# Performance work log

Hardware: AMD Instinct MI355X
Metric: run time of the kernel (lower is better)

The kernel has to match this reference:

```python
import jax, jax.numpy as jnp
import numpy as np

B, IN, OUT, TDIM, YDIM = 4096, 48, 64, 128, 64
HID = OUT * OUT  # 4096, Y_layer hidden/output width


def setup_inputs() -> dict:
    key = jax.random.key(0)
    ks = jax.random.split(key, 9)
    x = jax.random.normal(ks[0], (B, IN, IN), dtype=jnp.float32)
    # symmetrize so input is SPD-like (module assumes SPD inputs)
    x = 0.5 * (x + jnp.swapaxes(x, 1, 2))
    t = jax.random.normal(ks[1], (B, TDIM), dtype=jnp.float32)
    Y = jax.random.normal(ks[2], (B, YDIM), dtype=jnp.float32)
    # Stiefel (orthogonal) weight [input_size(=OUT after increase), output_size]
    W, _ = jnp.linalg.qr(jax.random.normal(ks[3], (OUT, OUT), dtype=jnp.float32))
    # Y_layer MLP params: Linear(YDIM,HID) -> SiLU -> Linear(HID,HID)
    Y_W1 = jax.random.normal(ks[4], (YDIM, HID), dtype=jnp.float32) / np.sqrt(YDIM)
    Y_b1 = jnp.zeros((HID,), dtype=jnp.float32)
    Y_W2 = jax.random.normal(ks[5], (HID, HID), dtype=jnp.float32) / np.sqrt(HID)
    Y_b2 = jnp.zeros((HID,), dtype=jnp.float32)
    return {"input": x, "t": t, "Y": Y, "W": W,
            "Y_W1": Y_W1, "Y_b1": Y_b1, "Y_W2": Y_W2, "Y_b2": Y_b2}


def reference(input, t, Y, W, Y_W1, Y_b1, Y_W2, Y_b2):
    # Y_layer MLP -> per-sample transform emb_Y [B, OUT, OUT]
    h = jax.nn.silu(Y @ Y_W1 + Y_b1)
    emb_Y = (h @ Y_W2 + Y_b2).reshape(B, OUT, OUT)
    # SPDIncreaseDim: embed input in top-left of OUTxOUT, ones on padded diagonal
    pad = OUT - IN
    xp = jnp.pad(input, ((0, 0), (0, pad), (0, pad)))
    add_diag = jnp.concatenate([jnp.zeros(IN, input.dtype), jnp.ones(pad, input.dtype)])
    xp = xp + jnp.diag(add_diag)[None]
    # congruence with Stiefel weight: W^T X W
    out = jnp.einsum('ji,bjk,kl->bil', W, xp, W)
    # congruence with MLP-generated weight: emb_Y X emb_Y^T
    out = jnp.einsum('bij,bjk,blk->bil', emb_Y, out, emb_Y)
    return out
```

## Files before the change

### kernel.cpp

```cpp
#include <hip/hip_runtime.h>
#include <hip/hip_bf16.h>

typedef __bf16 bf16;
typedef __bf16 bf16x8 __attribute__((ext_vector_type(8)));
typedef float floatx4 __attribute__((ext_vector_type(4)));

#define MFMA16(a, b, c) __builtin_amdgcn_mfma_f32_16x16x32_bf16((a), (b), (c), 0, 0, 0)

__device__ inline void gload_lds16(const void* g, void* l) {
    __builtin_amdgcn_global_load_lds((__attribute__((address_space(1))) void*)g,
                                     (__attribute__((address_space(3))) void*)l, 16, 0, 0);
}

__global__ __launch_bounds__(256) void prep_fused(
    const float* __restrict__ W2,
    const float* __restrict__ W,
    const float* __restrict__ b2,
    const float* __restrict__ Y,
    const float* __restrict__ W1,
    const float* __restrict__ b1,
    bf16* __restrict__ W2fT,
    float* __restrict__ b2f,
    bf16* __restrict__ h)
{
    __shared__ __align__(16) char smem[45056];
    int t = threadIdx.x, bid = blockIdx.x;
    int w = t >> 6, l = t & 63;
    int lm = l & 15, q2 = l >> 4, q8 = q2 * 8;

    if (bid < 2048) {
        int pt = bid & 31, i = bid >> 5;
        bf16* sW = (bf16*)smem;
        bf16* sA = sW + 64 * 72;
        bf16* sT = sA + 128 * 72;
        int p0 = pt * 128;

#pragma unroll
        for (int kk = 0; kk < 16; kk++) {
            int idx = t + 256 * kk;
            sW[(idx >> 6) * 72 + (idx & 63)] = (bf16)W[idx];
        }
        {
            const float* src = W2 + (size_t)p0 * 4096 + i * 64;
#pragma unroll
            for (int kk = 0; kk < 8; kk++) {
                int c = t + 256 * kk;
                int row = c >> 4, j4 = (c & 15) * 4;
                float4 v = *(const float4*)(src + (size_t)row * 4096 + j4);
                bf16 tmp[4] = {(bf16)v.x, (bf16)v.y, (bf16)v.z, (bf16)v.w};
                *(uint2*)(sA + row * 72 + j4) = *(const uint2*)tmp;
            }
        }
        __syncthreads();

        floatx4 acc[2][4] = {};
#pragma unroll
        for (int kc = 0; kc < 2; kc++) {
            bf16x8 a0 = *(const bf16x8*)(sA + (w * 32 + lm) * 72 + kc * 32 + q8);
            bf16x8 a1 = *(const bf16x8*)(sA + (w * 32 + 16 + lm) * 72 + kc * 32 + q8);
#pragma unroll
            for (int jn = 0; jn < 4; jn++) {
                bf16x8 bf_ = *(const bf16x8*)(sW + (jn * 16 + lm) * 72 + kc * 32 + q8);
                acc[0][jn] = MFMA16(a0, bf_, acc[0][jn]);
                acc[1][jn] = MFMA16(a1, bf_, acc[1][jn]);
            }
        }
#pragma unroll
        for (int im = 0; im < 2; im++)
#pragma unroll
            for (int jn = 0; jn < 4; jn++) {
                int pr = w * 32 + im * 16 + q2 * 4;
                int lc = jn * 16 + lm;
                union { bf16 h4[4]; uint2 u; } pk;
#pragma unroll
                for (int r = 0; r < 4; r++) pk.h4[r] = (bf16)acc[im][jn][r];
                *(uint2*)(sT + lc * 136 + pr) = pk.u;
            }
        __syncthreads();
#pragma unroll
        for (int kk = 0; kk < 4; kk++) {
            int c = t + 256 * kk;
            int row = c >> 4, off = (c & 15) * 8;
            uint4 v = *(const uint4*)(sT + row * 136 + off);
            *(uint4*)(W2fT + (size_t)(i * 64 + row) * 4096 + p0 + off) = v;
        }
        return;
    }

    if (bid < 2112) {
        int i = bid - 2048;
        if (t < 64) {
            float acc = 0.f;
            const float* b2r = b2 + i * 64;
            const float* wr_ = W + t * 64;
#pragma unroll
            for (int j = 0; j < 64; j++) acc = fmaf(b2r[j], wr_[j], acc);
            b2f[i * 64 + t] = acc;
        }
        return;
    }

    {
        int q = bid - 2112;
        int m0 = (q >> 5) * 128, n0 = (q & 31) * 128;
        bf16* sY = (bf16*)smem;
        bf16* sWT = sY + 128 * 72;

#pragma unroll
        for (int kk = 0; kk < 8; kk++) {
            int c = t + 256 * kk;
            int row = c >> 4, c4 = (c & 15) * 4;
            float4 v = *(const float4*)(Y + (size_t)(m0 + row) * 64 + c4);
            bf16 tmp[4] = {(bf16)v.x, (bf16)v.y, (bf16)v.z, (bf16)v.w};
            *(uint2*)(sY + row * 72 + c4) = *(const uint2*)tmp;
        }
#pragma unroll
        for (int kk = 0; kk < 8; kk++) {
            int c = t + 256 * kk;
            int k = c >> 5, j4 = (c & 31) * 4;
            float4 v = *(const float4*)(W1 + (size_t)k * 4096 + n0 + j4);
            sWT[(j4 + 0) * 72 + k] = (bf16)v.x;
            sWT[(j4 + 1) * 72 + k] = (bf16)v.y;
            sWT[(j4 + 2) * 72 + k] = (bf16)v.z;
            sWT[(j4 + 3) * 72 + k] = (bf16)v.w;
        }
        __syncthreads();

        int wn = (w & 1) * 64, wm = (w >> 1) * 64;
        floatx4 acc[4][4] = {};
#pragma unroll
        for (int kc = 0; kc < 2; kc++) {
            bf16x8 af[4], bfr[4];
#pragma unroll
            for (int i = 0; i < 4; i++)
                af[i] = *(const bf16x8*)(sWT + (wn + i * 16 + lm) * 72 + kc * 32 + q8);
#pragma unroll
            for (int j = 0; j < 4; j++)
                bfr[j] = *(const bf16x8*)(sY + (wm + j * 16 + lm) * 72 + kc * 32 + q8);
#pragma unroll
            for (int i = 0; i < 4; i++)
#pragma unroll
                for (int j = 0; j < 4; j++)
                    acc[i][j] = MFMA16(af[i], bfr[j], acc[i][j]);
        }
#pragma unroll
        for (int i = 0; i < 4; i++) {
            int nb = n0 + wn + i * 16 + q2 * 4;
            float4 bv = *(const float4*)(b1 + nb);
            float bb[4] = {bv.x, bv.y, bv.z, bv.w};
#pragma unroll
            for (int j = 0; j < 4; j++) {
                int m = m0 + wm + j * 16 + lm;
                union { bf16 h4[4]; uint2 u; } pk;
#pragma unroll
                for (int r = 0; r < 4; r++) {
                    float v = acc[i][j][r] + bb[r];
                    v = v / (1.f + __expf(-v));
                    pk.h4[r] = (bf16)v;
                }
                *(uint2*)(h + (size_t)m * 4096 + nb) = pk.u;
            }
        }
    }
}

#define GT 128
#define GK 32
__global__ __launch_bounds__(256, 4) void gemm_bt_bias(
    const bf16* __restrict__ A, const bf16* __restrict__ BT,
    const float* __restrict__ bias, bf16* __restrict__ C,
    int M, int N, int K)
{
    __shared__ bf16 sA[2][GT * GK];
    __shared__ bf16 sB[2][GT * GK];
    int t = threadIdx.x, w = t >> 6, l = t & 63;

    int bid = blockIdx.x;
    int xcd = bid & 7, local = bid >> 3;
    int mt = xcd * 4 + (local & 3);
    int nt = local >> 2;
    int m0 = mt * GT, n0 = nt * GT;

    int lm = l & 15;
    int q2 = l >> 4;
    int soff = ((q2 - (l & 3)) & 3) * 8;
    int wr = (w >> 1) * 64, wc = (w & 1) * 64;

    int rowA = (w * 64 + l) >> 2;
    int ko = (((l & 3) + rowA) & 3) * 8;
    const bf16* pa = A + (size_t)(m0 + rowA) * K + ko;
    const bf16* pb = BT + (size_t)(n0 + rowA) * K + ko;
    const int base0 = (w * 64) * 8, base1 = (w * 64 + 256) * 8;

    floatx4 acc[4][4] = {};

    auto issue = [&](int buf, const bf16* a, const bf16* b) {
        gload_lds16(a, &sA[buf][base0]);
        gload_lds16(a + (size_t)64 * K, &sA[buf][base1]);
        gload_lds16(b, &sB[buf][base0]);
        gload_lds16(b + (size_t)64 * K, &sB[buf][base1]);
    };

    const int KT = K / GK;
    issue(0, pa, pb);
    pa += GK; pb += GK;
    __syncthreads();

    for (int kt = 0; kt < KT; ++kt) {
        int cur = kt & 1;
        if (kt + 1 < KT) {
            issue(cur ^ 1, pa, pb);
            pa += GK; pb += GK;
        }
        const bf16* LA = sA[cur];
        const bf16* LB = sB[cur];
        bf16x8 af[4], bfr[4];
#pragma unroll
        for (int i = 0; i < 4; i++)
            af[i] = *(const bf16x8*)(LA + (wr + i * 16 + lm) * GK + soff);
#pragma unroll
        for (int j = 0; j < 4; j++)
            bfr[j] = *(const bf16x8*)(LB + (wc + j * 16 + lm) * GK + soff);
#pragma unroll
        for (int i = 0; i < 4; i++)
#pragma unroll
            for (int j = 0; j < 4; j++)
                acc[i][j] = MFMA16(af[i], bfr[j], acc[i][j]);
        __syncthreads();
    }

#pragma unroll
    for (int i = 0; i < 4; i++) {
        int r0 = m0 + wr + i * 16 + (l >> 4) * 4;
#pragma unroll
        for (int j = 0; j < 4; j++) {
            int cc = n0 + wc + j * 16 + lm;
            float bb = bias[cc];
#pragma unroll
            for (int r = 0; r < 4; r++)
                C[(size_t)(r0 + r) * N + cc] = (bf16)(acc[i][j][r] + bb);
        }
    }
}

#define ST 72
__global__ __launch_bounds__(256) void batched_congruence(
    const float* __restrict__ x,
    const bf16* __restrict__ F,
    float* __restrict__ out)
{
    __shared__ bf16 sX[64 * ST], sF[64 * ST], sT[64 * ST];
    int t = threadIdx.x, w = t >> 6, l = t & 63;
    int b = blockIdx.x;
    int lm = l & 15, q2 = l >> 4, q8 = q2 * 8;
    int r0 = (w >> 1) * 32, c0 = (w & 1) * 32;

    const float4* xb = (const float4*)(x + (size_t)b * 2304);
    float4 v0 = xb[t];
    float4 v1 = xb[t + 256];
    float4 v2 = (t < 64) ? xb[t + 512] : make_float4(0.f, 0.f, 0.f, 0.f);

    {
        const uint4* gf = (const uint4*)(F + (size_t)b * 4096);
#pragma unroll
        for (int kk = 0; kk < 2; kk++) {
            int c = t + 256 * kk;
            *(uint4*)(sF + (c >> 3) * ST + (c & 7) * 8) = gf[c];
        }
    }
    {
        unsigned* sx32 = (unsigned*)sX;
#pragma unroll
        for (int kk = 0; kk < 4; kk++) {
            int idx = t + 256 * kk;
            if (idx < 384) {
                int r = idx >> 3, d = 24 + (idx & 7);
                sx32[r * 36 + d] = 0u;
            } else if (idx < 896) {
                int k2 = idx - 384;
                int r = 48 + (k2 >> 5), d = k2 & 31;
                unsigned val = 0u;
                if (d == (r >> 1)) val = (r & 1) ? 0x3F800000u : 0x00003F80u;
                sx32[r * 36 + d] = val;
            }
        }
    }
    {
        int c = t;
        bf16 p4[4];
        p4[0] = (bf16)v0.x; p4[1] = (bf16)v0.y; p4[2] = (bf16)v0.z; p4[3] = (bf16)v0.w;
        *(uint2*)(sX + (c / 12) * ST + (c % 12) * 4) = *(const uint2*)p4;
        c = t + 256;
        p4[0] = (bf16)v1.x; p4[1] = (bf16)v1.y; p4[2] = (bf16)v1.z; p4[3] = (bf16)v1.w;
        *(uint2*)(sX + (c / 12) * ST + (c % 12) * 4) = *(const uint2*)p4;
        if (t < 64) {
            c = t + 512;
            p4[0] = (bf16)v2.x; p4[1] = (bf16)v2.y; p4[2] = (bf16)v2.z; p4[3] = (bf16)v2.w;
            *(uint2*)(sX + (c / 12) * ST + (c % 12) * 4) = *(const uint2*)p4;
        }
    }
    __syncthreads();

    auto mm = [&](const bf16* PA, const bf16* PB, floatx4 acc[2][2]) {
#pragma unroll
        for (int kc = 0; kc < 2; kc++) {
            bf16x8 a0 = *(const bf16x8*)(PA + (r0 + lm) * ST + kc * 32 + q8);
            bf16x8 a1 = *(const bf16x8*)(PA + (r0 + 16 + lm) * ST + kc * 32 + q8);
            bf16x8 b0 = *(const bf16x8*)(PB + (c0 + lm) * ST + kc * 32 + q8);
            bf16x8 b1 = *(const bf16x8*)(PB + (c0 + 16 + lm) * ST + kc * 32 + q8);
            acc[0][0] = MFMA16(a0, b0, acc[0][0]);
            acc[0][1] = MFMA16(a0, b1, acc[0][1]);
            acc[1][0] = MFMA16(a1, b0, acc[1][0]);
            acc[1][1] = MFMA16(a1, b1, acc[1][1]);
        }
    };

    floatx4 z = {0.f, 0.f, 0.f, 0.f};
    {
        floatx4 acc[2][2] = {{z, z}, {z, z}};
        mm(sX, sF, acc);
#pragma unroll
        for (int i = 0; i < 2; i++)
#pragma unroll
            for (int j = 0; j < 2; j++) {
                int R = r0 + i * 16 + q2 * 4;
                int Cc = c0 + j * 16 + lm;
                union { bf16 h4[4]; uint2 u; } pk;
#pragma unroll
                for (int r = 0; r < 4; r++) pk.h4[r] = (bf16)acc[i][j][r];
                *(uint2*)(sT + Cc * ST + R) = pk.u;
            }
    }
    __syncthreads();
    {
        floatx4 acc[2][2] = {{z, z}, {z, z}};
        mm(sT, sF, acc);
        float* ob = out + (size_t)b * 4096;
#pragma unroll
        for (int i = 0; i < 2; i++)
#pragma unroll
            for (int j = 0; j < 2; j++) {
                int R = r0 + i * 16 + q2 * 4;
                int Cc = c0 + j * 16 + lm;
#pragma unroll
                for (int r = 0; r < 4; r++)
                    out[(size_t)b * 4096 + (size_t)(R + r) * 64 + Cc] = acc[i][j][r];
            }
        (void)ob;
    }
}

extern "C" void kernel_launch(void* const* d_in, const int* in_sizes, int n_in,
                              void* d_out, int out_size, void* d_ws, size_t ws_size,
                              hipStream_t stream) {
    const float* x  = (const float*)d_in[0];
    const float* Y  = (const float*)d_in[2];
    const float* W  = (const float*)d_in[3];
    const float* W1 = (const float*)d_in[4];
    const float* b1 = (const float*)d_in[5];
    const float* W2 = (const float*)d_in[6];
    const float* b2 = (const float*)d_in[7];
    float* out = (float*)d_out;

    const size_t NN = (size_t)4096 * 4096;
    bf16* h    = (bf16*)d_ws;
    bf16* W2fT = h + NN;
    bf16* emb  = W2fT + NN;
    float* b2f = (float*)d_out;

    prep_fused<<<3136, 256, 0, stream>>>(W2, W, b2, Y, W1, b1, W2fT, b2f, h);
    gemm_bt_bias<<<1024, 256, 0, stream>>>(h, W2fT, b2f, emb, 4096, 4096, 4096);
    batched_congruence<<<4096, 256, 0, stream>>>(x, emb, out);
}
```

Baseline: 332.2 us.

## Fuse bias GEMM and batched congruence into one cooperative kernel with grid sync

Merges the large bf16 GEMM that produces the per-sample transforms and the per-sample congruence into one cooperative kernel, separated by a grid-wide sync. After the sync each block handles four samples and prefetches the next sample's input and transform while computing the current one. This removes a kernel launch and lets the congruence phase start right after the GEMM. The final output store becomes a vectorized transposed float4 write, which relies on the result being symmetric. It depends on all 1024 blocks being co-resident, and falls back to the two separate kernels if the cooperative launch fails.

```diff
diff --git a/kernel.cpp b/kernel.cpp
--- a/kernel.cpp
+++ b/kernel.cpp
@@ -1,5 +1,6 @@
 #include <hip/hip_runtime.h>
 #include <hip/hip_bf16.h>
+#include <hip/hip_cooperative_groups.h>
 
 typedef __bf16 bf16;
 typedef __bf16 bf16x8 __attribute__((ext_vector_type(8)));
@@ -12,16 +13,13 @@
                                      (__attribute__((address_space(3))) void*)l, 16, 0, 0);
 }
 
+#define ST 72
+
 __global__ __launch_bounds__(256) void prep_fused(
-    const float* __restrict__ W2,
-    const float* __restrict__ W,
-    const float* __restrict__ b2,
-    const float* __restrict__ Y,
-    const float* __restrict__ W1,
-    const float* __restrict__ b1,
-    bf16* __restrict__ W2fT,
-    float* __restrict__ b2f,
-    bf16* __restrict__ h)
+    const float* __restrict__ W2, const float* __restrict__ W,
+    const float* __restrict__ b2, const float* __restrict__ Y,
+    const float* __restrict__ W1, const float* __restrict__ b1,
+    bf16* __restrict__ W2fT, float* __restrict__ b2f, bf16* __restrict__ h)
 {
     __shared__ __align__(16) char smem[45056];
     int t = threadIdx.x, bid = blockIdx.x;
@@ -164,63 +162,239 @@
     }
 }
 
-#define GT 128
-#define GK 32
+__global__ __launch_bounds__(256, 4) void gemm_cong(
+    const bf16* __restrict__ A, const bf16* __restrict__ BT,
+    const float* __restrict__ bias, bf16* __restrict__ C,
+    const float* __restrict__ x, float* __restrict__ out)
+{
+    __shared__ __align__(16) char smem[32768];
+    int t = threadIdx.x, w = t >> 6, l = t & 63;
+    int bid = blockIdx.x;
+    int lm = l & 15, q2 = l >> 4, q8 = q2 * 8;
+
+    int s0 = bid * 4;
+    const float4* xb0 = (const float4*)(x + (size_t)s0 * 2304);
+    float4 v0 = xb0[t];
+    float4 v1 = xb0[t + 256];
+    float4 v2 = (t < 64) ? xb0[t + 512] : make_float4(0.f, 0.f, 0.f, 0.f);
+
+    {
+        bf16* sA = (bf16*)smem;
+        bf16* sB = (bf16*)(smem + 16384);
+        int xcd = bid & 7, local = bid >> 3;
+        int mt = xcd * 4 + (local & 3), nt = local >> 2;
+        int m0 = mt * 128, n0 = nt * 128;
+        int soff = ((q2 - (l & 3)) & 3) * 8;
+        int wr = (w >> 1) * 64, wc = (w & 1) * 64;
+        int rowA = (w * 64 + l) >> 2;
+        int ko = (((l & 3) + rowA) & 3) * 8;
+        const bf16* pa = A + (size_t)(m0 + rowA) * 4096 + ko;
+        const bf16* pb = BT + (size_t)(n0 + rowA) * 4096 + ko;
+        const int base0 = (w * 64) * 8, base1 = (w * 64 + 256) * 8;
+
+        floatx4 acc[4][4] = {};
+
+        auto issue = [&](int buf, const bf16* a, const bf16* b) {
+            gload_lds16(a, sA + buf * 4096 + base0);
+            gload_lds16(a + (size_t)64 * 4096, sA + buf * 4096 + base1);
+            gload_lds16(b, sB + buf * 4096 + base0);
+            gload_lds16(b + (size_t)64 * 4096, sB + buf * 4096 + base1);
+        };
+
+        issue(0, pa, pb);
+        pa += 32; pb += 32;
+        __syncthreads();
+
+        for (int kt = 0; kt < 128; ++kt) {
+            int cur = kt & 1;
+            if (kt + 1 < 128) {
+                issue(cur ^ 1, pa, pb);
+                pa += 32; pb += 32;
+            }
+            const bf16* LA = sA + cur * 4096;
+            const bf16* LB = sB + cur * 4096;
+            bf16x8 af[4], bfr[4];
+#pragma unroll
+            for (int i = 0; i < 4; i++)
+                af[i] = *(const bf16x8*)(LA + (wr + i * 16 + lm) * 32 + soff);
+#pragma unroll
+            for (int j = 0; j < 4; j++)
+                bfr[j] = *(const bf16x8*)(LB + (wc + j * 16 + lm) * 32 + soff);
+#pragma unroll
+            for (int i = 0; i < 4; i++)
+#pragma unroll
+                for (int j = 0; j < 4; j++)
+                    acc[i][j] = MFMA16(af[i], bfr[j], acc[i][j]);
+            __syncthreads();
+        }
+
+#pragma unroll
+        for (int i = 0; i < 4; i++) {
+            int r0g = m0 + wr + i * 16 + q2 * 4;
+#pragma unroll
+            for (int j = 0; j < 4; j++) {
+                int cc = n0 + wc + j * 16 + lm;
+                float bb = bias[cc];
+#pragma unroll
+                for (int r = 0; r < 4; r++)
+                    C[(size_t)(r0g + r) * 4096 + cc] = (bf16)(acc[i][j][r] + bb);
+            }
+        }
+    }
+
+    __threadfence();
+    cooperative_groups::this_grid().sync();
+
+    {
+        bf16* sX = (bf16*)smem;
+        bf16* sF = (bf16*)(smem + 9216);
+        bf16* sT = (bf16*)(smem + 18432);
+        int r0 = (w >> 1) * 32, c0 = (w & 1) * 32;
+
+        const uint4* gf0 = (const uint4*)(C + (size_t)s0 * 4096);
+        uint4 f0 = gf0[t], f1 = gf0[t + 256];
+
+        auto mm = [&](const bf16* PA, const bf16* PB, floatx4 acc2[2][2]) {
+#pragma unroll
+            for (int kc = 0; kc < 2; kc++) {
+                bf16x8 a0 = *(const bf16x8*)(PA + (r0 + lm) * ST + kc * 32 + q8);
+                bf16x8 a1 = *(const bf16x8*)(PA + (r0 + 16 + lm) * ST + kc * 32 + q8);
+                bf16x8 b0 = *(const bf16x8*)(PB + (c0 + lm) * ST + kc * 32 + q8);
+                bf16x8 b1 = *(const bf16x8*)(PB + (c0 + 16 + lm) * ST + kc * 32 + q8);
+                acc2[0][0] = MFMA16(a0, b0, acc2[0][0]);
+                acc2[0][1] = MFMA16(a0, b1, acc2[0][1]);
+                acc2[1][0] = MFMA16(a1, b0, acc2[1][0]);
+                acc2[1][1] = MFMA16(a1, b1, acc2[1][1]);
+            }
+        };
+
+        for (int s = 0; s < 4; ++s) {
+            {
+                int c = t;
+                *(uint4*)(sF + (c >> 3) * ST + (c & 7) * 8) = f0;
+                c = t + 256;
+                *(uint4*)(sF + (c >> 3) * ST + (c & 7) * 8) = f1;
+            }
+            {
+                unsigned* sx32 = (unsigned*)sX;
+#pragma unroll
+                for (int kk = 0; kk < 4; kk++) {
+                    int idx = t + 256 * kk;
+                    if (idx < 384) {
+                        int r = idx >> 3, d = 24 + (idx & 7);
+                        sx32[r * 36 + d] = 0u;
+                    } else if (idx < 896) {
+                        int k2 = idx - 384;
+                        int r = 48 + (k2 >> 5), d = k2 & 31;
+                        unsigned val = 0u;
+                        if (d == (r >> 1)) val = (r & 1) ? 0x3F800000u : 0x00003F80u;
+                        sx32[r * 36 + d] = val;
+                    }
+                }
+            }
+            {
+                int c = t;
+                bf16 p4[4];
+                p4[0] = (bf16)v0.x; p4[1] = (bf16)v0.y; p4[2] = (bf16)v0.z; p4[3] = (bf16)v0.w;
+                *(uint2*)(sX + (c / 12) * ST + (c % 12) * 4) = *(const uint2*)p4;
+                c = t + 256;
+                p4[0] = (bf16)v1.x; p4[1] = (bf16)v1.y; p4[2] = (bf16)v1.z; p4[3] = (bf16)v1.w;
+                *(uint2*)(sX + (c / 12) * ST + (c % 12) * 4) = *(const uint2*)p4;
+                if (t < 64) {
+                    c = t + 512;
+                    p4[0] = (bf16)v2.x; p4[1] = (bf16)v2.y; p4[2] = (bf16)v2.z; p4[3] = (bf16)v2.w;
+                    *(uint2*)(sX + (c / 12) * ST + (c % 12) * 4) = *(const uint2*)p4;
+                }
+            }
+            __syncthreads();
+
+            if (s < 3) {
+                const float4* xb = (const float4*)(x + (size_t)(s0 + s + 1) * 2304);
+                v0 = xb[t]; v1 = xb[t + 256];
+                if (t < 64) v2 = xb[t + 512];
+                const uint4* gf = (const uint4*)(C + (size_t)(s0 + s + 1) * 4096);
+                f0 = gf[t]; f1 = gf[t + 256];
+            }
+
+            floatx4 z = {0.f, 0.f, 0.f, 0.f};
+            {
+                floatx4 a2[2][2] = {{z, z}, {z, z}};
+                mm(sX, sF, a2);
+#pragma unroll
+                for (int i = 0; i < 2; i++)
+#pragma unroll
+                    for (int j = 0; j < 2; j++) {
+                        int R = r0 + i * 16 + q2 * 4;
+                        int Cc = c0 + j * 16 + lm;
+                        union { bf16 h4[4]; uint2 u; } pk;
+#pragma unroll
+                        for (int r = 0; r < 4; r++) pk.h4[r] = (bf16)a2[i][j][r];
+                        *(uint2*)(sT + Cc * ST + R) = pk.u;
+                    }
+            }
+            __syncthreads();
+            {
+                floatx4 a3[2][2] = {{z, z}, {z, z}};
+                mm(sT, sF, a3);
+                float* ob = out + (size_t)(s0 + s) * 4096;
+#pragma unroll
+                for (int i = 0; i < 2; i++)
+#pragma unroll
+                    for (int j = 0; j < 2; j++) {
+                        int R = r0 + i * 16 + q2 * 4;
+                        int Cc = c0 + j * 16 + lm;
+                        float4 vout = make_float4(a3[i][j][0], a3[i][j][1],
+                                                  a3[i][j][2], a3[i][j][3]);
+                        *(float4*)(ob + Cc * 64 + R) = vout;
+                    }
+            }
+            __syncthreads();
+        }
+    }
+}
+
 __global__ __launch_bounds__(256, 4) void gemm_bt_bias(
     const bf16* __restrict__ A, const bf16* __restrict__ BT,
-    const float* __restrict__ bias, bf16* __restrict__ C,
-    int M, int N, int K)
+    const float* __restrict__ bias, bf16* __restrict__ C)
 {
-    __shared__ bf16 sA[2][GT * GK];
-    __shared__ bf16 sB[2][GT * GK];
+    __shared__ bf16 sA[2][4096];
+    __shared__ bf16 sB[2][4096];
     int t = threadIdx.x, w = t >> 6, l = t & 63;
-
     int bid = blockIdx.x;
     int xcd = bid & 7, local = bid >> 3;
-    int mt = xcd * 4 + (local & 3);
-    int nt = local >> 2;
-    int m0 = mt * GT, n0 = nt * GT;
-
-    int lm = l & 15;
-    int q2 = l >> 4;
+    int mt = xcd * 4 + (local & 3), nt = local >> 2;
+    int m0 = mt * 128, n0 = nt * 128;
+    int lm = l & 15, q2 = l >> 4;
     int soff = ((q2 - (l & 3)) & 3) * 8;
     int wr = (w >> 1) * 64, wc = (w & 1) * 64;
-
     int rowA = (w * 64 + l) >> 2;
     int ko = (((l & 3) + rowA) & 3) * 8;
-    const bf16* pa = A + (size_t)(m0 + rowA) * K + ko;
-    const bf16* pb = BT + (size_t)(n0 + rowA) * K + ko;
+    const bf16* pa = A + (size_t)(m0 + rowA) * 4096 + ko;
+    const bf16* pb = BT + (size_t)(n0 + rowA) * 4096 + ko;
     const int base0 = (w * 64) * 8, base1 = (w * 64 + 256) * 8;
 
     floatx4 acc[4][4] = {};
-
     auto issue = [&](int buf, const bf16* a, const bf16* b) {
         gload_lds16(a, &sA[buf][base0]);
-        gload_lds16(a + (size_t)64 * K, &sA[buf][base1]);
+        gload_lds16(a + (size_t)64 * 4096, &sA[buf][base1]);
         gload_lds16(b, &sB[buf][base0]);
-        gload_lds16(b + (size_t)64 * K, &sB[buf][base1]);
+        gload_lds16(b + (size_t)64 * 4096, &sB[buf][base1]);
     };
-
-    const int KT = K / GK;
     issue(0, pa, pb);
-    pa += GK; pb += GK;
+    pa += 32; pb += 32;
     __syncthreads();
-
-    for (int kt = 0; kt < KT; ++kt) {
+    for (int kt = 0; kt < 128; ++kt) {
         int cur = kt & 1;
-        if (kt + 1 < KT) {
-            issue(cur ^ 1, pa, pb);
-            pa += GK; pb += GK;
-        }
+        if (kt + 1 < 128) { issue(cur ^ 1, pa, pb); pa += 32; pb += 32; }
         const bf16* LA = sA[cur];
         const bf16* LB = sB[cur];
         bf16x8 af[4], bfr[4];
 #pragma unroll
         for (int i = 0; i < 4; i++)
-            af[i] = *(const bf16x8*)(LA + (wr + i * 16 + lm) * GK + soff);
+            af[i] = *(const bf16x8*)(LA + (wr + i * 16 + lm) * 32 + soff);
 #pragma unroll
         for (int j = 0; j < 4; j++)
-            bfr[j] = *(const bf16x8*)(LB + (wc + j * 16 + lm) * GK + soff);
+            bfr[j] = *(const bf16x8*)(LB + (wc + j * 16 + lm) * 32 + soff);
 #pragma unroll
         for (int i = 0; i < 4; i++)
 #pragma unroll
@@ -228,25 +402,22 @@
                 acc[i][j] = MFMA16(af[i], bfr[j], acc[i][j]);
         __syncthreads();
     }
-
 #pragma unroll
     for (int i = 0; i < 4; i++) {
-        int r0 = m0 + wr + i * 16 + (l >> 4) * 4;
+        int r0 = m0 + wr + i * 16 + q2 * 4;
 #pragma unroll
         for (int j = 0; j < 4; j++) {
             int cc = n0 + wc + j * 16 + lm;
             float bb = bias[cc];
 #pragma unroll
             for (int r = 0; r < 4; r++)
-                C[(size_t)(r0 + r) * N + cc] = (bf16)(acc[i][j][r] + bb);
+                C[(size_t)(r0 + r) * 4096 + cc] = (bf16)(acc[i][j][r] + bb);
         }
     }
 }
 
-#define ST 72
 __global__ __launch_bounds__(256) void batched_congruence(
-    const float* __restrict__ x,
-    const bf16* __restrict__ F,
+    const float* __restrict__ x, const bf16* __restrict__ F,
     float* __restrict__ out)
 {
     __shared__ bf16 sX[64 * ST], sF[64 * ST], sT[64 * ST];
@@ -259,7 +430,6 @@
     float4 v0 = xb[t];
     float4 v1 = xb[t + 256];
     float4 v2 = (t < 64) ? xb[t + 512] : make_float4(0.f, 0.f, 0.f, 0.f);
-
     {
         const uint4* gf = (const uint4*)(F + (size_t)b * 4096);
 #pragma unroll
@@ -317,8 +487,8 @@
 
     floatx4 z = {0.f, 0.f, 0.f, 0.f};
     {
-        floatx4 acc[2][2] = {{z, z}, {z, z}};
-        mm(sX, sF, acc);
+        floatx4 a2[2][2] = {{z, z}, {z, z}};
+        mm(sX, sF, a2);
 #pragma unroll
         for (int i = 0; i < 2; i++)
 #pragma unroll
@@ -327,14 +497,14 @@
                 int Cc = c0 + j * 16 + lm;
                 union { bf16 h4[4]; uint2 u; } pk;
 #pragma unroll
-                for (int r = 0; r < 4; r++) pk.h4[r] = (bf16)acc[i][j][r];
+                for (int r = 0; r < 4; r++) pk.h4[r] = (bf16)a2[i][j][r];
                 *(uint2*)(sT + Cc * ST + R) = pk.u;
             }
     }
     __syncthreads();
     {
-        floatx4 acc[2][2] = {{z, z}, {z, z}};
-        mm(sT, sF, acc);
+        floatx4 a3[2][2] = {{z, z}, {z, z}};
+        mm(sT, sF, a3);
         float* ob = out + (size_t)b * 4096;
 #pragma unroll
         for (int i = 0; i < 2; i++)
@@ -342,11 +512,9 @@
             for (int j = 0; j < 2; j++) {
                 int R = r0 + i * 16 + q2 * 4;
                 int Cc = c0 + j * 16 + lm;
-#pragma unroll
-                for (int r = 0; r < 4; r++)
-                    out[(size_t)b * 4096 + (size_t)(R + r) * 64 + Cc] = acc[i][j][r];
-            }
-        (void)ob;
+                float4 vout = make_float4(a3[i][j][0], a3[i][j][1], a3[i][j][2], a3[i][j][3]);
+                *(float4*)(ob + Cc * 64 + R) = vout;
+            }
     }
 }
 
@@ -369,6 +537,14 @@
     float* b2f = (float*)d_out;
 
     prep_fused<<<3136, 256, 0, stream>>>(W2, W, b2, Y, W1, b1, W2fT, b2f, h);
-    gemm_bt_bias<<<1024, 256, 0, stream>>>(h, W2fT, b2f, emb, 4096, 4096, 4096);
-    batched_congruence<<<4096, 256, 0, stream>>>(x, emb, out);
+
+    const bf16* hA = h; const bf16* bB = W2fT; const float* bb = b2f;
+    bf16* cC = emb; const float* xx = x; float* oo = out;
+    void* cargs[6] = {(void*)&hA, (void*)&bB, (void*)&bb, (void*)&cC, (void*)&xx, (void*)&oo};
+    hipError_t err = hipLaunchCooperativeKernel((const void*)gemm_cong,
+                                                dim3(1024), dim3(256), cargs, 0, stream);
+    if (err != hipSuccess) {
+        gemm_bt_bias<<<1024, 256, 0, stream>>>(h, W2fT, b2f, emb);
+        batched_congruence<<<4096, 256, 0, stream>>>(x, emb, out);
+    }
 }
```

New measurement: 648.0 us. 1.95x slower.
